# Performance work log

Hardware: AMD Instinct MI355X
Metric: run time of the kernel (lower is better)

The kernel has to match this reference:

```python
import jax, jax.numpy as jnp
import numpy as np
import math

B, SQ, SK, D, H = 2, 2048, 2048, 1024, 16
DH = D // H
EPS = 1e-5

def _ln(x, g, b):
    m = jnp.mean(x, axis=-1, keepdims=True)
    v = jnp.mean(jnp.square(x - m), axis=-1, keepdims=True)
    return (x - m) / jnp.sqrt(v + EPS) * g + b

def setup_inputs() -> dict:
    key = jax.random.key(0)
    ks = jax.random.split(key, 8)
    xav = math.sqrt(6.0 / (D + D))  # xavier_uniform for square [D,D] weights
    inp = {
        'Q': jax.random.normal(ks[0], (B, SQ, D), dtype=jnp.float32),
        'K': jax.random.normal(ks[1], (B, SK, D), dtype=jnp.float32),
        'pad_mask': jax.random.randint(ks[2], (B, SK), 0, 2, dtype=jnp.int32),
        'Wq': jax.random.uniform(ks[3], (D, D), jnp.float32, -xav, xav),
        'Wk': jax.random.uniform(ks[4], (D, D), jnp.float32, -xav, xav),
        'Wv': jax.random.uniform(ks[5], (D, D), jnp.float32, -xav, xav),
        'Wo': jax.random.uniform(ks[6], (D, D), jnp.float32, -xav, xav),
        'bq': jnp.zeros((D,), jnp.float32),
        'bk': jnp.zeros((D,), jnp.float32),
        'bv': jnp.zeros((D,), jnp.float32),
        'bo': jnp.zeros((D,), jnp.float32),
        'ln_q_g': jnp.ones((D,), jnp.float32),  'ln_q_b': jnp.zeros((D,), jnp.float32),
        'ln_kv_g': jnp.ones((D,), jnp.float32), 'ln_kv_b': jnp.zeros((D,), jnp.float32),
        'ln_f_g': jnp.ones((D,), jnp.float32),  'ln_f_b': jnp.zeros((D,), jnp.float32),
    }
    return inp

def reference(Q, K, pad_mask, Wq, Wk, Wv, Wo, bq, bk, bv, bo,
              ln_q_g, ln_q_b, ln_kv_g, ln_kv_b, ln_f_g, ln_f_b):
    Q_ = _ln(Q, ln_q_g, ln_q_b)
    K_ = _ln(K, ln_kv_g, ln_kv_b)
    # projections (PyTorch Linear: x @ W.T + b)
    Q1 = (Q_ @ Wq.T + bq).reshape(B, SQ, H, DH)
    K1 = (K_ @ Wk.T + bk).reshape(B, SK, H, DH)
    V1 = (K_ @ Wv.T + bv).reshape(B, SK, H, DH)
    # note: scaling uses sqrt(dim_V), NOT sqrt(head_dim), per source
    score = jnp.einsum('bqhd,bkhd->bhqk', Q1, K1) / math.sqrt(D)
    m = pad_mask[:, None, None, :]  # [B,1,1,SK]
    score = jnp.where(m == 0, jnp.float32(-1e12), score)
    A = jax.nn.softmax(score, axis=-1)
    A = A * m.astype(A.dtype)  # second mask application after softmax
    O1 = jnp.einsum('bhqk,bkhd->bqhd', A, V1).reshape(B, SQ, D)
    O2 = jax.nn.relu(Q_ @ Wo.T + bo)
    return _ln(Q + O1 + O2, ln_f_g, ln_f_b)
```

## Files before the change

kernel.cpp:

```cpp
#include <hip/hip_runtime.h>
#include <stdint.h>

#define NB 2
#define NSQ 2048
#define NSK 2048
#define ND 1024
#define NH 16
#define NDH 64

typedef unsigned short u16;
typedef unsigned int u32;
typedef __bf16 bf16x8_t __attribute__((ext_vector_type(8)));
typedef float f32x4_t __attribute__((ext_vector_type(4)));
typedef u32 u32x4_t __attribute__((ext_vector_type(4)));
typedef short s16x4 __attribute__((ext_vector_type(4)));
typedef u32 u32x2_t __attribute__((ext_vector_type(2)));

#define AS1 __attribute__((address_space(1)))
#define AS3 __attribute__((address_space(3)))

__device__ __forceinline__ float bf2f(u16 u) {
    union { float f; u32 i; } v; v.i = ((u32)u) << 16; return v.f;
}
__device__ __forceinline__ u16 f2bf(float x) {
    union { float f; u32 i; } v; v.f = x;
    u32 r = v.i + 0x7fffu + ((v.i >> 16) & 1u);
    return (u16)(r >> 16);
}
__device__ __forceinline__ u32 fbits(float x) {
    union { float f; u32 i; } v; v.f = x; return v.i;
}
__device__ __forceinline__ float fexp2(float x) {
#if __has_builtin(__builtin_amdgcn_exp2f)
    return __builtin_amdgcn_exp2f(x);
#else
    return exp2f(x);
#endif
}
__device__ __forceinline__ f32x4_t mfma16(s16x4 a, s16x4 b, f32x4_t c) {
#if __has_builtin(__builtin_amdgcn_mfma_f32_16x16x16bf16_1k)
    return __builtin_amdgcn_mfma_f32_16x16x16bf16_1k(a, b, c, 0, 0, 0);
#else
    asm("v_mfma_f32_16x16x16_bf16 %0, %1, %2, %0" : "+v"(c) : "v"(a), "v"(b));
    return c;
#endif
}
__device__ __forceinline__ int detect_f32(const u16* __restrict__ Q) {
    uint2 x = ((const uint2*)Q)[threadIdx.x & 63];
    u16 a0 = x.x & 0xffff, a1 = x.x >> 16, a2 = x.y & 0xffff, a3 = x.y >> 16;
    bool big = (((a0 >> 7) & 0xff) >= 0x8D) || (((a1 >> 7) & 0xff) >= 0x8D) ||
               (((a2 >> 7) & 0xff) >= 0x8D) || (((a3 >> 7) & 0xff) >= 0x8D);
    return __any(big);
}

#define PREP_LN   (2 * NB * NSQ)
#define PREP_CVT  4106
__global__ __launch_bounds__(256) void prep_kernel(
    const void* __restrict__ Q, const void* __restrict__ K,
    const int* __restrict__ pad_mask,
    const void* __restrict__ Wq, const void* __restrict__ Wk,
    const void* __restrict__ Wv, const void* __restrict__ Wo,
    const void* __restrict__ vbq, const void* __restrict__ vbk,
    const void* __restrict__ vbv, const void* __restrict__ vbo,
    const void* __restrict__ g0, const void* __restrict__ b0,
    const void* __restrict__ g1, const void* __restrict__ b1,
    const void* __restrict__ g2, const void* __restrict__ b2,
    u16* __restrict__ Wc, u16* __restrict__ Vc,
    int* __restrict__ idx, int* __restrict__ cnt,
    u16* __restrict__ Qn, u16* __restrict__ Kn)
{
    int bx = blockIdx.x;
    int t  = threadIdx.x;

    if (bx < PREP_LN) {
        int flag = detect_f32((const u16*)Q);
        int row = bx;
        const void* x; const void *gv, *bv; u16* y;
        size_t roff;
        if (row < NB * NSQ) {
            x = Q; roff = (size_t)row * ND;
            gv = g0; bv = b0;
            y = Qn + roff;
        } else {
            int r2 = row - NB * NSQ;
            x = K; roff = (size_t)r2 * ND;
            gv = g1; bv = b1;
            y = Kn + roff;
        }
        float v0, v1, v2, v3, gg0, gg1, gg2, gg3, bb0, bb1, bb2, bb3;
        if (flag) {
            float4 xv = ((const float4*)x)[roff / 4 + t];
            v0 = xv.x; v1 = xv.y; v2 = xv.z; v3 = xv.w;
            float4 G = ((const float4*)gv)[t];
            float4 Bv = ((const float4*)bv)[t];
            gg0 = G.x; gg1 = G.y; gg2 = G.z; gg3 = G.w;
            bb0 = Bv.x; bb1 = Bv.y; bb2 = Bv.z; bb3 = Bv.w;
        } else {
            uint2 ux = ((const uint2*)x)[roff / 4 + t];
            v0 = bf2f(ux.x & 0xffff); v1 = bf2f(ux.x >> 16);
            v2 = bf2f(ux.y & 0xffff); v3 = bf2f(ux.y >> 16);
            uint2 G = ((const uint2*)gv)[t];
            uint2 Bv = ((const uint2*)bv)[t];
            gg0 = bf2f(G.x & 0xffff); gg1 = bf2f(G.x >> 16);
            gg2 = bf2f(G.y & 0xffff); gg3 = bf2f(G.y >> 16);
            bb0 = bf2f(Bv.x & 0xffff); bb1 = bf2f(Bv.x >> 16);
            bb2 = bf2f(Bv.y & 0xffff); bb3 = bf2f(Bv.y >> 16);
        }
        float s1 = v0 + v1 + v2 + v3;
        float s2 = v0*v0 + v1*v1 + v2*v2 + v3*v3;
#pragma unroll
        for (int off = 32; off >= 1; off >>= 1) {
            s1 += __shfl_xor(s1, off);
            s2 += __shfl_xor(s2, off);
        }
        __shared__ float r1[4], r2[4];
        int wave = t >> 6;
        if ((t & 63) == 0) { r1[wave] = s1; r2[wave] = s2; }
        __syncthreads();
        float t1 = r1[0] + r1[1] + r1[2] + r1[3];
        float t2 = r2[0] + r2[1] + r2[2] + r2[3];
        float mean = t1 * (1.0f / ND);
        float var  = t2 * (1.0f / ND) - mean * mean;
        float rstd = rsqrtf(var + 1e-5f);
        float y0 = (v0 - mean) * rstd * gg0 + bb0;
        float y1 = (v1 - mean) * rstd * gg1 + bb1;
        float y2 = (v2 - mean) * rstd * gg2 + bb2;
        float y3 = (v3 - mean) * rstd * gg3 + bb3;
        uint2 o;
        o.x = (u32)f2bf(y0) | ((u32)f2bf(y1) << 16);
        o.y = (u32)f2bf(y2) | ((u32)f2bf(y3) << 16);
        ((uint2*)y)[t] = o;
    } else if (bx < PREP_LN + PREP_CVT) {
        int flag = detect_f32((const u16*)Q);
        int blk = bx - PREP_LN;
        const void* src;
        u16* dst;
        size_t srcoff;
        if (blk < 4096) {
            int w = blk >> 10;
            src = (w == 0) ? Wq : (w == 1) ? Wk : (w == 2) ? Wv : Wo;
            srcoff = (size_t)(blk & 1023) * 1024;
            dst = Wc + (size_t)w * 1024 * 1024 + srcoff;
        } else {
            int v = blk - 4096;
            src = (v == 0) ? vbq : (v == 1) ? vbk : (v == 2) ? vbv : (v == 3) ? vbo :
                  (v == 4) ? g0  : (v == 5) ? b0  : (v == 6) ? g1  : (v == 7) ? b1 :
                  (v == 8) ? g2  : b2;
            srcoff = 0;
            dst = Vc + (size_t)v * 1024;
        }
        u32 lo, hi;
        if (flag) {
            float4 x = ((const float4*)src)[srcoff / 4 + t];
            lo = (u32)f2bf(x.x) | ((u32)f2bf(x.y) << 16);
            hi = (u32)f2bf(x.z) | ((u32)f2bf(x.w) << 16);
        } else {
            uint2 x = ((const uint2*)src)[srcoff / 4 + t];
            lo = x.x; hi = x.y;
        }
        uint2 o; o.x = lo; o.y = hi;
        ((uint2*)dst)[t] = o;
    } else {
        int b = bx - (PREP_LN + PREP_CVT);
        const int* m = pad_mask + b * NSK;
        int loc[8]; int s = 0;
#pragma unroll
        for (int i = 0; i < 8; ++i) { loc[i] = (m[t * 8 + i] != 0); s += loc[i]; }
        __shared__ int ps[256];
        ps[t] = s;
        __syncthreads();
        for (int off = 1; off < 256; off <<= 1) {
            int v = (t >= off) ? ps[t - off] : 0;
            __syncthreads();
            ps[t] += v;
            __syncthreads();
        }
        int run = ps[t] - s;
#pragma unroll
        for (int i = 0; i < 8; ++i)
            if (loc[i]) idx[b * NSK + run++] = t * 8 + i;
        if (t == 255) cnt[b] = ps[255];
    }
}

__global__ __launch_bounds__(512, 2) void gemm4_kernel(
    const u16* __restrict__ Qn, const u16* __restrict__ Kn,
    const u16* __restrict__ Wc, const u16* __restrict__ Vc,
    u16* __restrict__ Q1, u16* __restrict__ K1, u16* __restrict__ V1,
    u16* __restrict__ R)
{
    int lin = blockIdx.x + 16 * blockIdx.y + 64 * blockIdx.z;
    int u   = (lin & 7) * 32 + (lin >> 3);
    int bx  = u & 15;
    int by  = (u >> 4) & 3;
    int z   = u >> 6;

    const u16* X    = (z == 0 || z == 3) ? Qn : Kn;
    const u16* W    = Wc + (size_t)z * 1024 * 1024;
    const u16* bias = Vc + (size_t)z * 1024;

    __shared__ u16 sm[4][2][256 * 32];

    int tid  = threadIdx.x;
    int wave = tid >> 6, lane = tid & 63;
    int wm = wave >> 2, wn = wave & 3;
    int quad = lane >> 4, l4 = lane & 15;
    int m0 = bx * 256;
    int n0 = by * 256;

    int srow   = wave * 16 + (lane >> 2);
    int schunk = (lane & 3) ^ ((srow >> 1) & 3);
    const u16* gA = X + (size_t)(m0 + srow) * ND + schunk * 8;
    const u16* gB = W + (size_t)(n0 + srow) * ND + schunk * 8;

#define STAGE_A(t_) do { int s_ = (t_) & 3; \
    __builtin_amdgcn_global_load_lds((const AS1 u32*)(gA + (t_) * 32), \
        (AS3 u32*)(&sm[s_][0][wave * 512]), 16, 0, 0); \
    __builtin_amdgcn_global_load_lds((const AS1 u32*)(gA + (t_) * 32 + (size_t)128 * ND), \
        (AS3 u32*)(&sm[s_][0][4096 + wave * 512]), 16, 0, 0); \
} while (0)
#define STAGE_B(t_) do { int s_ = (t_) & 3; \
    __builtin_amdgcn_global_load_lds((const AS1 u32*)(gB + (t_) * 32), \
        (AS3 u32*)(&sm[s_][1][wave * 512]), 16, 0, 0); \
    __builtin_amdgcn_global_load_lds((const AS1 u32*)(gB + (t_) * 32 + (size_t)128 * ND), \
        (AS3 u32*)(&sm[s_][1][4096 + wave * 512]), 16, 0, 0); \
} while (0)

    int fch   = (quad ^ ((l4 >> 1) & 3)) * 8;
    int aoffb = (wm * 128 + l4) * 32 + fch;
    int boffb = (wn * 64  + l4) * 32 + fch;

    f32x4_t acc[8][4];
#pragma unroll
    for (int i = 0; i < 8; ++i)
#pragma unroll
        for (int j = 0; j < 4; ++j)
            acc[i][j] = (f32x4_t){0.f, 0.f, 0.f, 0.f};

    STAGE_A(0); STAGE_B(0);
    STAGE_A(1); STAGE_B(1);
    STAGE_A(2); STAGE_B(2);
    asm volatile("s_waitcnt vmcnt(8)" ::: "memory");
    __builtin_amdgcn_s_barrier();
    __builtin_amdgcn_sched_barrier(0);

    for (int t = 0; t < 32; ++t) {
        const u16* a = &sm[t & 3][0][0];
        const u16* b = &sm[t & 3][1][0];
        bf16x8_t bf[4], af[4], ah[4];

#pragma unroll
        for (int nf = 0; nf < 4; ++nf)
            bf[nf] = *(const bf16x8_t*)(b + boffb + nf * 512);
#pragma unroll
        for (int mf = 0; mf < 4; ++mf)
            af[mf] = *(const bf16x8_t*)(a + aoffb + mf * 512);
#pragma unroll
        for (int mf = 0; mf < 4; ++mf)
            ah[mf] = *(const bf16x8_t*)(a + aoffb + (mf + 4) * 512);

        if (t < 29) { STAGE_A(t + 3); STAGE_B(t + 3); }

        __builtin_amdgcn_s_setprio(1);
#pragma unroll
        for (int mf = 0; mf < 4; ++mf)
#pragma unroll
            for (int nf = 0; nf < 4; ++nf)
                acc[mf][nf] = __builtin_amdgcn_mfma_f32_16x16x32_bf16(
                    af[mf], bf[nf], acc[mf][nf], 0, 0, 0);
#pragma unroll
        for (int mf = 0; mf < 4; ++mf)
#pragma unroll
            for (int nf = 0; nf < 4; ++nf)
                acc[mf + 4][nf] = __builtin_amdgcn_mfma_f32_16x16x32_bf16(
                    ah[mf], bf[nf], acc[mf + 4][nf], 0, 0, 0);
        __builtin_amdgcn_s_setprio(0);

        if (t < 29)       asm volatile("s_waitcnt vmcnt(8)" ::: "memory");
        else if (t == 29) asm volatile("s_waitcnt vmcnt(4)" ::: "memory");
        else if (t == 30) asm volatile("s_waitcnt vmcnt(0)" ::: "memory");
        __builtin_amdgcn_s_barrier();
        __builtin_amdgcn_sched_barrier(0);
    }
#undef STAGE_A
#undef STAGE_B

    u16* outp = (z == 0) ? Q1 : (z == 1) ? K1 : (z == 2) ? V1 : R;
    float bv_[4];
#pragma unroll
    for (int nf = 0; nf < 4; ++nf)
        bv_[nf] = bf2f(bias[n0 + wn * 64 + nf * 16 + l4]);
#pragma unroll
    for (int mf = 0; mf < 8; ++mf) {
#pragma unroll
        for (int r = 0; r < 4; ++r) {
            int m = m0 + wm * 128 + mf * 16 + quad * 4 + r;
#pragma unroll
            for (int nf = 0; nf < 4; ++nf) {
                int n = n0 + wn * 64 + nf * 16 + l4;
                float val = acc[mf][nf][r] + bv_[nf];
                if (z == 0) val *= 0.045105964f;
                if (z == 3) val = fmaxf(val, 0.f);
                outp[(size_t)m * ND + n] = f2bf(val);
            }
        }
    }
}

__global__ __launch_bounds__(256) void gather_kernel(
    const u16* __restrict__ K1, const u16* __restrict__ V1,
    const int* __restrict__ idx, const int* __restrict__ cnt,
    u16* __restrict__ Kc, u16* __restrict__ Vct)
{
    int b = blockIdx.y;
    int c = cnt[b];
    int cPad = (c + 63) & ~63;
    int tid = threadIdx.x;

    if (blockIdx.x < 128) {
        int jb = blockIdx.x * 16;
        if (jb >= cPad) return;
        int row = tid >> 4;
        int seg = tid & 15;
        int j = jb + row;
        if (j >= cPad) return;
        bool z = (j >= c);
        const u16* src = z ? (const u16*)0
            : K1 + ((size_t)b * NSK + idx[(size_t)b * NSK + j]) * ND;
        u16* dst = Kc + ((size_t)b * NSK + j) * ND;
#pragma unroll
        for (int i = 0; i < 8; ++i) {
            int off = (seg * 8 + i) * 8;
            uint4 v = z ? (uint4){0, 0, 0, 0} : *(const uint4*)(src + off);
            *(uint4*)(dst + off) = v;
        }
    } else {
        int lin = blockIdx.x - 128;
        int kb = lin & 31;
        int h  = lin >> 5;
        if (kb * 64 >= cPad) return;
        __shared__ u16 sT[64 * 72];
        {
            int row = tid >> 3, seg = tid & 7;
            int j1 = kb * 64 + row, j2 = j1 + 32;
            uint4 v1 = {0, 0, 0, 0}, v2 = {0, 0, 0, 0};
            if (j1 < c) v1 = *(const uint4*)(V1 +
                ((size_t)b * NSK + idx[(size_t)b * NSK + j1]) * ND + h * NDH + seg * 8);
            if (j2 < c) v2 = *(const uint4*)(V1 +
                ((size_t)b * NSK + idx[(size_t)b * NSK + j2]) * ND + h * NDH + seg * 8);
            *(uint4*)(sT + row * 72 + seg * 8) = v1;
            *(uint4*)(sT + (row + 32) * 72 + seg * 8) = v2;
        }
        __syncthreads();
        int d = tid >> 2, sg = tid & 3;
        u16 buf[16];
#pragma unroll
        for (int i = 0; i < 8; ++i) buf[i]     = sT[(sg * 8 + i) * 72 + d];
#pragma unroll
        for (int i = 0; i < 8; ++i) buf[8 + i] = sT[((sg + 4) * 8 + i) * 72 + d];
        u16* go = Vct + ((size_t)(b * NH + h) * NDH + d) * NSK + kb * 64;
        *(uint4*)(go + sg * 8)       = *(uint4*)buf;
        *(uint4*)(go + (sg + 4) * 8) = *(uint4*)(buf + 8);
    }
}

__global__ __launch_bounds__(256, 4) void attn_kernel(
    const u16* __restrict__ Q1, const u16* __restrict__ Kc,
    const u16* __restrict__ Vct, const int* __restrict__ cnt,
    u16* __restrict__ R)
{
    int q0 = blockIdx.x * 64;
    int h  = blockIdx.y;
    int b  = blockIdx.z;

    __shared__ u16 sK[2][64 * 64];
    __shared__ u16 sV[2][64 * 64];

    int tid  = threadIdx.x;
    int wave = tid >> 6, lane = tid & 63;
    int quad = lane >> 4, l4 = lane & 15;
    int lk = lane >> 3, ls = lane & 7;
    int gseg = ls ^ lk;

    int c  = cnt[b];
    int nt = (c + 63) >> 6;

    bf16x8_t qf[2];
    {
        const u16* qp = Q1 + (size_t)(b * NSQ + q0 + wave * 16 + l4) * ND + h * NDH;
        qf[0] = *(const bf16x8_t*)(qp + quad * 8);
        qf[1] = *(const bf16x8_t*)(qp + 32 + quad * 8);
    }

    const u16* kbase = Kc + (size_t)b * NSK * ND + h * NDH;
    const u16* vbase = Vct + (size_t)(b * NH + h) * NDH * NSK;

    const u16* gk0 = kbase + (size_t)(wave * 16 + lk) * ND + gseg * 8;
    const u16* gk1 = gk0 + (size_t)8 * ND;
    const u16* gv0 = vbase + (size_t)(wave * 16 + lk) * NSK + gseg * 8;
    const u16* gv1 = gv0 + (size_t)8 * NSK;

    int fragOff[2];
#pragma unroll
    for (int kk = 0; kk < 2; ++kk)
        fragOff[kk] = l4 * 64 + (((kk * 4 + quad) ^ (l4 & 7)) * 8);

    int v4off[4];
#pragma unroll
    for (int tm = 0; tm < 4; ++tm)
        v4off[tm] = l4 * 64 + (((2 * tm + (quad >> 1)) ^ (l4 & 7)) * 8)
                  + (quad & 1) * 4;

    float l_run = 0.f;
    f32x4_t acc_o[4];
#pragma unroll
    for (int T = 0; T < 4; ++T) acc_o[T] = (f32x4_t){0.f, 0.f, 0.f, 0.f};

    if (nt > 0) {
        __builtin_amdgcn_global_load_lds((const AS1 u32*)gk0,
            (AS3 u32*)(&sK[0][(wave * 16) * 64]), 16, 0, 0);
        __builtin_amdgcn_global_load_lds((const AS1 u32*)gk1,
            (AS3 u32*)(&sK[0][(wave * 16 + 8) * 64]), 16, 0, 0);
        __builtin_amdgcn_global_load_lds((const AS1 u32*)gv0,
            (AS3 u32*)(&sV[0][(wave * 16) * 64]), 16, 0, 0);
        __builtin_amdgcn_global_load_lds((const AS1 u32*)gv1,
            (AS3 u32*)(&sV[0][(wave * 16 + 8) * 64]), 16, 0, 0);
        gk0 += (size_t)64 * ND; gk1 += (size_t)64 * ND;
        gv0 += 64; gv1 += 64;

        for (int kb = 0; kb < nt; ++kb) {
            __syncthreads();

            if (kb + 1 < nt) {
                int bi = (kb + 1) & 1;
                __builtin_amdgcn_global_load_lds((const AS1 u32*)gk0,
                    (AS3 u32*)(&sK[bi][(wave * 16) * 64]), 16, 0, 0);
                __builtin_amdgcn_global_load_lds((const AS1 u32*)gk1,
                    (AS3 u32*)(&sK[bi][(wave * 16 + 8) * 64]), 16, 0, 0);
                __builtin_amdgcn_global_load_lds((const AS1 u32*)gv0,
                    (AS3 u32*)(&sV[bi][(wave * 16) * 64]), 16, 0, 0);
                __builtin_amdgcn_global_load_lds((const AS1 u32*)gv1,
                    (AS3 u32*)(&sV[bi][(wave * 16 + 8) * 64]), 16, 0, 0);
                gk0 += (size_t)64 * ND; gk1 += (size_t)64 * ND;
                gv0 += 64; gv1 += 64;
            }

            const u16* kt = sK[kb & 1];
            const u16* vt = sV[kb & 1];

            f32x4_t accs[4];
            if (kb == nt - 1) {
#pragma unroll
                for (int tm = 0; tm < 4; ++tm) {
                    int key = kb * 64 + tm * 16 + quad * 4;
#pragma unroll
                    for (int r = 0; r < 4; ++r)
                        accs[tm][r] = (key + r < c) ? 0.f : -1e9f;
                }
            } else {
#pragma unroll
                for (int tm = 0; tm < 4; ++tm)
                    accs[tm] = (f32x4_t){0.f, 0.f, 0.f, 0.f};
            }
#pragma unroll
            for (int kk = 0; kk < 2; ++kk)
#pragma unroll
                for (int tm = 0; tm < 4; ++tm) {
                    bf16x8_t kf = *(const bf16x8_t*)(kt + tm * 1024 + fragOff[kk]);
                    accs[tm] = __builtin_amdgcn_mfma_f32_16x16x32_bf16(
                        kf, qf[kk], accs[tm], 0, 0, 0);
                }

            float lsum = 0.f;
#pragma unroll
            for (int tm = 0; tm < 4; ++tm) {
                float p0 = fexp2(accs[tm][0]);
                float p1 = fexp2(accs[tm][1]);
                float p2 = fexp2(accs[tm][2]);
                float p3 = fexp2(accs[tm][3]);
                lsum += (p0 + p1) + (p2 + p3);
                u32 lo = __builtin_amdgcn_perm(fbits(p1), fbits(p0), 0x07060302);
                u32 hi = __builtin_amdgcn_perm(fbits(p3), fbits(p2), 0x07060302);
                s16x4 pf = __builtin_bit_cast(s16x4, (u32x2_t){lo, hi});
#pragma unroll
                for (int T = 0; T < 4; ++T) {
                    s16x4 vf = *(const s16x4*)(vt + T * 1024 + v4off[tm]);
                    acc_o[T] = mfma16(vf, pf, acc_o[T]);
                }
            }
            lsum += __shfl_xor(lsum, 16);
            lsum += __shfl_xor(lsum, 32);
            l_run += lsum;
        }
    }

    float inv = l_run > 0.f ? 1.f / l_run : 0.f;
    u16* rp = R + (size_t)(b * NSQ + q0 + wave * 16 + l4) * ND + h * NDH;
#pragma unroll
    for (int T = 0; T < 4; ++T) {
        u16* p = rp + T * 16 + quad * 4;
        uint2 o2 = *(const uint2*)p;
        float e0 = acc_o[T][0] * inv + bf2f(o2.x & 0xffff);
        float e1 = acc_o[T][1] * inv + bf2f(o2.x >> 16);
        float e2 = acc_o[T][2] * inv + bf2f(o2.y & 0xffff);
        float e3 = acc_o[T][3] * inv + bf2f(o2.y >> 16);
        uint2 on;
        on.x = (u32)f2bf(e0) | ((u32)f2bf(e1) << 16);
        on.y = (u32)f2bf(e2) | ((u32)f2bf(e3) << 16);
        *(uint2*)p = on;
    }
}

__global__ __launch_bounds__(256) void ln_out_kernel(
    const void* __restrict__ Q, const u16* __restrict__ R,
    const u16* __restrict__ Vc, void* __restrict__ out)
{
    int row = blockIdx.x;
    size_t roff = (size_t)row * ND;
    int t = threadIdx.x;
    int f = detect_f32((const u16*)Q);
    float v0, v1, v2, v3;
    uint2 ur = ((const uint2*)(R + roff))[t];
    if (f) {
        float4 xq = ((const float4*)Q)[roff / 4 + t];
        v0 = xq.x; v1 = xq.y; v2 = xq.z; v3 = xq.w;
    } else {
        uint2 uq = ((const uint2*)Q)[roff / 4 + t];
        v0 = bf2f(uq.x & 0xffff); v1 = bf2f(uq.x >> 16);
        v2 = bf2f(uq.y & 0xffff); v3 = bf2f(uq.y >> 16);
    }
    v0 += bf2f(ur.x & 0xffff); v1 += bf2f(ur.x >> 16);
    v2 += bf2f(ur.y & 0xffff); v3 += bf2f(ur.y >> 16);
    float s1 = v0 + v1 + v2 + v3;
    float s2 = v0*v0 + v1*v1 + v2*v2 + v3*v3;
#pragma unroll
    for (int off = 32; off >= 1; off >>= 1) {
        s1 += __shfl_xor(s1, off);
        s2 += __shfl_xor(s2, off);
    }
    __shared__ float r1[4], r2[4];
    int wave = t >> 6;
    if ((t & 63) == 0) { r1[wave] = s1; r2[wave] = s2; }
    __syncthreads();
    float t1 = r1[0] + r1[1] + r1[2] + r1[3];
    float t2 = r2[0] + r2[1] + r2[2] + r2[3];
    float mean = t1 * (1.0f / ND);
    float var  = t2 * (1.0f / ND) - mean * mean;
    float rstd = rsqrtf(var + 1e-5f);
    const u16* g  = Vc + 8 * 1024;
    const u16* bb = Vc + 9 * 1024;
    uint2 ug = ((const uint2*)g)[t];
    uint2 ub = ((const uint2*)bb)[t];
    float y0 = (v0 - mean) * rstd * bf2f(ug.x & 0xffff) + bf2f(ub.x & 0xffff);
    float y1 = (v1 - mean) * rstd * bf2f(ug.x >> 16)    + bf2f(ub.x >> 16);
    float y2 = (v2 - mean) * rstd * bf2f(ug.y & 0xffff) + bf2f(ub.y & 0xffff);
    float y3 = (v3 - mean) * rstd * bf2f(ug.y >> 16)    + bf2f(ub.y >> 16);
    if (f) {
        float4 o; o.x = y0; o.y = y1; o.z = y2; o.w = y3;
        ((float4*)out)[roff / 4 + t] = o;
    } else {
        uint2 o;
        o.x = (u32)f2bf(y0) | ((u32)f2bf(y1) << 16);
        o.y = (u32)f2bf(y2) | ((u32)f2bf(y3) << 16);
        ((uint2*)out)[roff / 4 + t] = o;
    }
}

extern "C" void kernel_launch(void* const* d_in, const int* in_sizes, int n_in,
                              void* d_out, int out_size, void* d_ws, size_t ws_size,
                              hipStream_t stream) {
    const void* Q        = d_in[0];
    const void* K        = d_in[1];
    const int* pad_mask  = (const int*)d_in[2];

    const size_t NEL = (size_t)NB * NSQ * ND;
    int* flag = (int*)d_ws;
    int* cnt  = flag + 1;
    int* idx  = flag + 4;
    u16* base = (u16*)(idx + 4096);
    u16* Qn  = base;
    u16* Kn  = Qn + NEL;
    u16* Q1  = Kn + NEL;
    u16* K1  = Q1 + NEL;
    u16* V1  = K1 + NEL;
    u16* R   = V1 + NEL;
    u16* Wc  = R + NEL;
    u16* Vc  = Wc + (size_t)4 * 1024 * 1024;
    u16* Kc  = Qn;
    u16* Vct = Kn;

    prep_kernel<<<dim3(PREP_LN + PREP_CVT + NB), dim3(256), 0, stream>>>(
        Q, K, pad_mask,
        d_in[3], d_in[4], d_in[5], d_in[6],
        d_in[7], d_in[8], d_in[9], d_in[10],
        d_in[11], d_in[12], d_in[13], d_in[14], d_in[15], d_in[16],
        Wc, Vc, idx, cnt, Qn, Kn);

    gemm4_kernel<<<dim3(16, 4, 4), dim3(512), 0, stream>>>(
        Qn, Kn, Wc, Vc, Q1, K1, V1, R);

    gather_kernel<<<dim3(128 + 32 * NH, NB), dim3(256), 0, stream>>>(
        K1, V1, idx, cnt, Kc, Vct);

    attn_kernel<<<dim3(NSQ / 64, NH, NB), dim3(256), 0, stream>>>(
        Q1, Kc, Vct, cnt, R);

    ln_out_kernel<<<dim3(NB * NSQ), dim3(256), 0, stream>>>(
        Q, R, Vc, d_out);
}
```

Baseline: 213.7 us.

## Fuse key compaction gather and V transpose into projection GEMM

The K and V projection tiles now load their A rows through the compacted index list, so only unmasked keys are projected and K1 comes out already compacted. Tiles wholly past the padded count exit early. The V tile is stored transposed straight into the Vct layout, which removes the separate gather kernel launch and its extra read/write of K1 and V1. The cost is scattered row addresses in the GEMM A loads and strided transposed stores in the V epilogue.

```diff
diff --git a/kernel.cpp b/kernel.cpp
--- a/kernel.cpp
+++ b/kernel.cpp
@@ -186,7 +186,8 @@
 __global__ __launch_bounds__(512, 2) void gemm4_kernel(
     const u16* __restrict__ Qn, const u16* __restrict__ Kn,
     const u16* __restrict__ Wc, const u16* __restrict__ Vc,
-    u16* __restrict__ Q1, u16* __restrict__ K1, u16* __restrict__ V1,
+    const int* __restrict__ cnt, const int* __restrict__ idx,
+    u16* __restrict__ Q1, u16* __restrict__ K1, u16* __restrict__ Vct,
     u16* __restrict__ R)
 {
     int lin = blockIdx.x + 16 * blockIdx.y + 64 * blockIdx.z;
@@ -195,6 +196,15 @@
     int by  = (u >> 4) & 3;
     int z   = u >> 6;
 
+    int kv = (z == 1 || z == 2);
+    int batch = bx >> 3;
+    int c2 = 0;
+    if (kv) {
+        c2 = cnt[batch];
+        int cPad = (c2 + 63) & ~63;
+        if ((bx & 7) * 256 >= cPad) return;
+    }
+
     const u16* X    = (z == 0 || z == 3) ? Qn : Kn;
     const u16* W    = Wc + (size_t)z * 1024 * 1024;
     const u16* bias = Vc + (size_t)z * 1024;
@@ -210,13 +220,24 @@
 
     int srow   = wave * 16 + (lane >> 2);
     int schunk = (lane & 3) ^ ((srow >> 1) & 3);
-    const u16* gA = X + (size_t)(m0 + srow) * ND + schunk * 8;
+    const u16 *gA0, *gA1;
+    if (kv) {
+        int jg0 = (bx & 7) * 256 + srow;
+        int jg1 = jg0 + 128;
+        int ar0 = (jg0 < c2) ? idx[batch * NSK + jg0] : 0;
+        int ar1 = (jg1 < c2) ? idx[batch * NSK + jg1] : 0;
+        gA0 = Kn + ((size_t)batch * NSK + ar0) * ND + schunk * 8;
+        gA1 = Kn + ((size_t)batch * NSK + ar1) * ND + schunk * 8;
+    } else {
+        gA0 = X + (size_t)(m0 + srow) * ND + schunk * 8;
+        gA1 = gA0 + (size_t)128 * ND;
+    }
     const u16* gB = W + (size_t)(n0 + srow) * ND + schunk * 8;
 
 #define STAGE_A(t_) do { int s_ = (t_) & 3; \
-    __builtin_amdgcn_global_load_lds((const AS1 u32*)(gA + (t_) * 32), \
+    __builtin_amdgcn_global_load_lds((const AS1 u32*)(gA0 + (t_) * 32), \
         (AS3 u32*)(&sm[s_][0][wave * 512]), 16, 0, 0); \
-    __builtin_amdgcn_global_load_lds((const AS1 u32*)(gA + (t_) * 32 + (size_t)128 * ND), \
+    __builtin_amdgcn_global_load_lds((const AS1 u32*)(gA1 + (t_) * 32), \
         (AS3 u32*)(&sm[s_][0][4096 + wave * 512]), 16, 0, 0); \
 } while (0)
 #define STAGE_B(t_) do { int s_ = (t_) & 3; \
@@ -285,11 +306,33 @@
 #undef STAGE_A
 #undef STAGE_B
 
-    u16* outp = (z == 0) ? Q1 : (z == 1) ? K1 : (z == 2) ? V1 : R;
     float bv_[4];
 #pragma unroll
     for (int nf = 0; nf < 4; ++nf)
         bv_[nf] = bf2f(bias[n0 + wn * 64 + nf * 16 + l4]);
+
+    if (z == 2) {
+        int jb = (bx & 7) * 256 + wm * 128;
+#pragma unroll
+        for (int nf = 0; nf < 4; ++nf) {
+            int n = n0 + wn * 64 + nf * 16 + l4;
+            float bvv = bv_[nf];
+            u16* rowp = Vct + ((size_t)batch * 1024 + n) * NSK;
+#pragma unroll
+            for (int mf = 0; mf < 8; ++mf) {
+                int j = jb + mf * 16 + quad * 4;
+                uint2 o;
+                o.x = (u32)f2bf(acc[mf][nf][0] + bvv)
+                    | ((u32)f2bf(acc[mf][nf][1] + bvv) << 16);
+                o.y = (u32)f2bf(acc[mf][nf][2] + bvv)
+                    | ((u32)f2bf(acc[mf][nf][3] + bvv) << 16);
+                *(uint2*)(rowp + j) = o;
+            }
+        }
+        return;
+    }
+
+    u16* outp = (z == 0) ? Q1 : (z == 1) ? K1 : R;
 #pragma unroll
     for (int mf = 0; mf < 8; ++mf) {
 #pragma unroll
@@ -307,65 +350,8 @@
     }
 }
 
-__global__ __launch_bounds__(256) void gather_kernel(
-    const u16* __restrict__ K1, const u16* __restrict__ V1,
-    const int* __restrict__ idx, const int* __restrict__ cnt,
-    u16* __restrict__ Kc, u16* __restrict__ Vct)
-{
-    int b = blockIdx.y;
-    int c = cnt[b];
-    int cPad = (c + 63) & ~63;
-    int tid = threadIdx.x;
-
-    if (blockIdx.x < 128) {
-        int jb = blockIdx.x * 16;
-        if (jb >= cPad) return;
-        int row = tid >> 4;
-        int seg = tid & 15;
-        int j = jb + row;
-        if (j >= cPad) return;
-        bool z = (j >= c);
-        const u16* src = z ? (const u16*)0
-            : K1 + ((size_t)b * NSK + idx[(size_t)b * NSK + j]) * ND;
-        u16* dst = Kc + ((size_t)b * NSK + j) * ND;
-#pragma unroll
-        for (int i = 0; i < 8; ++i) {
-            int off = (seg * 8 + i) * 8;
-            uint4 v = z ? (uint4){0, 0, 0, 0} : *(const uint4*)(src + off);
-            *(uint4*)(dst + off) = v;
-        }
-    } else {
-        int lin = blockIdx.x - 128;
-        int kb = lin & 31;
-        int h  = lin >> 5;
-        if (kb * 64 >= cPad) return;
-        __shared__ u16 sT[64 * 72];
-        {
-            int row = tid >> 3, seg = tid & 7;
-            int j1 = kb * 64 + row, j2 = j1 + 32;
-            uint4 v1 = {0, 0, 0, 0}, v2 = {0, 0, 0, 0};
-            if (j1 < c) v1 = *(const uint4*)(V1 +
-                ((size_t)b * NSK + idx[(size_t)b * NSK + j1]) * ND + h * NDH + seg * 8);
-            if (j2 < c) v2 = *(const uint4*)(V1 +
-                ((size_t)b * NSK + idx[(size_t)b * NSK + j2]) * ND + h * NDH + seg * 8);
-            *(uint4*)(sT + row * 72 + seg * 8) = v1;
-            *(uint4*)(sT + (row + 32) * 72 + seg * 8) = v2;
-        }
-        __syncthreads();
-        int d = tid >> 2, sg = tid & 3;
-        u16 buf[16];
-#pragma unroll
-        for (int i = 0; i < 8; ++i) buf[i]     = sT[(sg * 8 + i) * 72 + d];
-#pragma unroll
-        for (int i = 0; i < 8; ++i) buf[8 + i] = sT[((sg + 4) * 8 + i) * 72 + d];
-        u16* go = Vct + ((size_t)(b * NH + h) * NDH + d) * NSK + kb * 64;
-        *(uint4*)(go + sg * 8)       = *(uint4*)buf;
-        *(uint4*)(go + (sg + 4) * 8) = *(uint4*)(buf + 8);
-    }
-}
-
 __global__ __launch_bounds__(256, 4) void attn_kernel(
-    const u16* __restrict__ Q1, const u16* __restrict__ Kc,
+    const u16* __restrict__ Q1, const u16* __restrict__ K1c,
     const u16* __restrict__ Vct, const int* __restrict__ cnt,
     u16* __restrict__ R)
 {
@@ -392,7 +378,7 @@
         qf[1] = *(const bf16x8_t*)(qp + 32 + quad * 8);
     }
 
-    const u16* kbase = Kc + (size_t)b * NSK * ND + h * NDH;
+    const u16* kbase = K1c + (size_t)b * NSK * ND + h * NDH;
     const u16* vbase = Vct + (size_t)(b * NH + h) * NDH * NSK;
 
     const u16* gk0 = kbase + (size_t)(wave * 16 + lk) * ND + gseg * 8;
@@ -582,12 +568,10 @@
     u16* Kn  = Qn + NEL;
     u16* Q1  = Kn + NEL;
     u16* K1  = Q1 + NEL;
-    u16* V1  = K1 + NEL;
-    u16* R   = V1 + NEL;
+    u16* Vct = K1 + NEL;
+    u16* R   = Vct + NEL;
     u16* Wc  = R + NEL;
     u16* Vc  = Wc + (size_t)4 * 1024 * 1024;
-    u16* Kc  = Qn;
-    u16* Vct = Kn;
 
     prep_kernel<<<dim3(PREP_LN + PREP_CVT + NB), dim3(256), 0, stream>>>(
         Q, K, pad_mask,
@@ -597,13 +581,10 @@
         Wc, Vc, idx, cnt, Qn, Kn);
 
     gemm4_kernel<<<dim3(16, 4, 4), dim3(512), 0, stream>>>(
-        Qn, Kn, Wc, Vc, Q1, K1, V1, R);
-
-    gather_kernel<<<dim3(128 + 32 * NH, NB), dim3(256), 0, stream>>>(
-        K1, V1, idx, cnt, Kc, Vct);
+        Qn, Kn, Wc, Vc, cnt, idx, Q1, K1, Vct, R);
 
     attn_kernel<<<dim3(NSQ / 64, NH, NB), dim3(256), 0, stream>>>(
-        Q1, Kc, Vct, cnt, R);
+        Q1, K1, Vct, cnt, R);
 
     ln_out_kernel<<<dim3(NB * NSQ), dim3(256), 0, stream>>>(
         Q, R, Vc, d_out);
```

Result: faster. 206.9 us (-3.2%).
